# Kernel optimization log

Measured on AMD Instinct MI355X. Metric: run time of the kernel, lower is better.

Reference implementation:

```python
import jax, jax.numpy as jnp
import numpy as np

NUM_TASKS, IN_SIZE, OUT_SIZE, N_ROWS = 64, 512, 512, 2048


def setup_inputs() -> dict:
    key = jax.random.key(0)
    k_x, k_t, k_w = jax.random.split(key, 3)
    inputs = jax.random.normal(k_x, (N_ROWS, IN_SIZE), dtype=jnp.float32)
    task_ids = jax.random.randint(k_t, (N_ROWS,), 0, NUM_TASKS, dtype=jnp.int64)
    # in_size == out_size path: identity + N(0, 0.03) perturbation per task
    W = (jnp.eye(IN_SIZE, OUT_SIZE, dtype=jnp.float32)[None]
         + 0.03 * jax.random.normal(k_w, (NUM_TASKS, IN_SIZE, OUT_SIZE), dtype=jnp.float32))
    return {"inputs": inputs, "task_ids": task_ids, "W": W}


def reference(inputs, task_ids, W):
    # Gather the full per-row weight matrix then batched vector-matrix multiply,
    # faithful to torch.einsum('ni,nio->no', inputs, W[task_ids]).
    aligned = W[task_ids]                       # [I, in, out]
    return jnp.einsum("ni,nio->no", inputs, aligned)  # [I, out]
```

## Files before the change

### kernel.cpp

```cpp
#include <hip/hip_runtime.h>


#define NDIM 512
#define KDIM 512
#define NCOL 32

typedef _Float16 f16x8 __attribute__((ext_vector_type(8)));
typedef float    f32x4 __attribute__((ext_vector_type(4)));

__global__ __launch_bounds__(256) void k_fused(
    const float* __restrict__ x,
    const int*   __restrict__ tids,
    const float* __restrict__ W,
    float*       __restrict__ out,
    int n_rows)
{
    const int tid  = threadIdx.x;
    const int lane = tid & 63;
    const int wv   = tid >> 6;
    const int c0   = blockIdx.x * NCOL;
    const int task = blockIdx.y;

    __shared__ __align__(16) _Float16 Wt[NCOL * KDIM];
    __shared__ unsigned short rlw[4 * 128];
    __shared__ unsigned short rl[256];
    __shared__ int wcnt[4];

    int trow[8], tval[8];
    #pragma unroll
    for (int it = 0; it < 8; ++it) {
        trow[it] = wv * 512 + it * 64 + lane;
        tval[it] = (trow[it] < n_rows) ? tids[trow[it]] : -1;
    }

    const int sc4   = (tid & 7) * 4;
    const int obase = tid >> 3;
    const float* Wg = W + (size_t)task * KDIM * NDIM + c0;
    float4 wr[16];
    #pragma unroll
    for (int j = 0; j < 8; ++j)
        wr[j] = *(const float4*)(Wg + (size_t)(obase * 8 + j) * NDIM + sc4);
    #pragma unroll
    for (int j = 0; j < 8; ++j)
        wr[8 + j] = *(const float4*)(Wg + (size_t)((obase + 32) * 8 + j) * NDIM + sc4);

    int cloc = 0;
    #pragma unroll
    for (int it = 0; it < 8; ++it) {
        const bool m = (tval[it] == task);
        const unsigned long long bal = __ballot(m);
        const int rank = __popcll(bal & ((1ull << lane) - 1ull));
        if (m) rlw[wv * 128 + cloc + rank] = (unsigned short)trow[it];
        cloc += __popcll(bal);
    }
    if (lane == 0) wcnt[wv] = cloc;

    #pragma unroll
    for (int h = 0; h < 2; ++h) {
        const int oct = obase + h * 32;
        #pragma unroll
        for (int j2 = 0; j2 < 4; ++j2) {
            f16x8 h8;
            #pragma unroll
            for (int j = 0; j < 8; ++j)
                h8[j] = (_Float16)(((const float*)&wr[h * 8 + j])[j2]);
            const int c  = sc4 + j2;
            const int po = oct ^ (c & 7);
            *(f16x8*)&Wt[c * KDIM + po * 8] = h8;
        }
    }

    __syncthreads();

    const int n0 = wcnt[0], n1 = wcnt[1], n2 = wcnt[2], n3 = wcnt[3];
    const int o1 = n0, o2 = n0 + n1, o3 = o2 + n2;
    const int count = o3 + n3;
    if (tid < count && tid < 256) {
        int w, base;
        if (tid < o1)      { w = 0; base = 0;  }
        else if (tid < o2) { w = 1; base = o1; }
        else if (tid < o3) { w = 2; base = o2; }
        else               { w = 3; base = o3; }
        rl[tid] = rlw[w * 128 + tid - base];
    }
    __syncthreads();

    if (count == 0) return;

    const int ml = lane & 15;
    const int q  = lane >> 4;

    for (int g0 = 0; g0 < count; g0 += 64) {
        const int rr = g0 + wv * 16 + ml;
        const int rowid = rl[(rr < count) ? rr : 0];
        const float* xrow = x + (size_t)rowid * KDIM;

        f32x4 acc[2] = {};
        #pragma unroll
        for (int p = 0; p < 2; ++p) {
            const int kb = p * 256;
            float4 xa[16];
            #pragma unroll
            for (int ks = 0; ks < 8; ++ks) {
                xa[2 * ks]     = *(const float4*)(xrow + kb + ks * 32 + q * 8);
                xa[2 * ks + 1] = *(const float4*)(xrow + kb + ks * 32 + q * 8 + 4);
            }
            #pragma unroll
            for (int ks = 0; ks < 8; ++ks) {
                f16x8 af;
                const float* a0 = (const float*)&xa[2 * ks];
                #pragma unroll
                for (int j = 0; j < 8; ++j) af[j] = (_Float16)a0[j];
                #pragma unroll
                for (int ct = 0; ct < 2; ++ct) {
                    const int cB = ct * 16 + ml;
                    const int po = (p * 32 + ks * 4 + q) ^ (cB & 7);
                    const f16x8 bf = *(const f16x8*)&Wt[cB * KDIM + po * 8];
                    acc[ct] = __builtin_amdgcn_mfma_f32_16x16x32_f16(af, bf, acc[ct], 0, 0, 0);
                }
            }
        }

        #pragma unroll
        for (int rg = 0; rg < 4; ++rg) {
            const int rr2 = g0 + wv * 16 + q * 4 + rg;
            if (rr2 < count) {
                float* op = out + (size_t)rl[rr2] * NDIM + c0 + ml;
                op[0]  = acc[0][rg];
                op[16] = acc[1][rg];
            }
        }
    }
}

extern "C" void kernel_launch(void* const* d_in, const int* in_sizes, int n_in,
                              void* d_out, int out_size, void* d_ws, size_t ws_size,
                              hipStream_t stream) {
    const float* x    = (const float*)d_in[0];
    const int*   tids = (const int*)d_in[1];
    const float* W    = (const float*)d_in[2];
    float*       out  = (float*)d_out;
    const int n_rows  = in_sizes[1];

    k_fused<<<dim3(NDIM / NCOL, 64), dim3(256), 0, stream>>>(x, tids, W, out, n_rows);
}
```

Measured before the change: 108.4 us.

## Pipeline W chunk staging with per-wave row lists and prefetched activations

The W tile is split into two 16-column chunks staged one after the other, with the second chunk's global loads overlapping the MFMA work on the first. Each wave now keeps its own matched-row list, which removes the cross-wave compaction pass and one block barrier. Task ids are read with vectorized loads, activations are converted to fp16 fragments once and reused for both chunks, and launch bounds request higher occupancy. In exchange, MFMA work is spread unevenly across waves, since each wave processes only its own matched rows.

```diff
diff --git a/kernel.cpp b/kernel.cpp
--- a/kernel.cpp
+++ b/kernel.cpp
@@ -3,12 +3,14 @@
 
 #define NDIM 512
 #define KDIM 512
-#define NCOL 32
+#define CCH  16
+#define NCH  2
 
 typedef _Float16 f16x8 __attribute__((ext_vector_type(8)));
 typedef float    f32x4 __attribute__((ext_vector_type(4)));
+typedef int      i32x4 __attribute__((ext_vector_type(4)));
 
-__global__ __launch_bounds__(256) void k_fused(
+__global__ __launch_bounds__(256, 4) void k_fused2(
     const float* __restrict__ x,
     const int*   __restrict__ tids,
     const float* __restrict__ W,
@@ -18,92 +20,59 @@
     const int tid  = threadIdx.x;
     const int lane = tid & 63;
     const int wv   = tid >> 6;
-    const int c0   = blockIdx.x * NCOL;
+    const int c0   = blockIdx.x * (CCH * NCH);
     const int task = blockIdx.y;
 
-    __shared__ __align__(16) _Float16 Wt[NCOL * KDIM];
+    __shared__ __align__(16) _Float16 Wt[NCH][CCH * KDIM];
     __shared__ unsigned short rlw[4 * 128];
-    __shared__ unsigned short rl[256];
-    __shared__ int wcnt[4];
 
-    int trow[8], tval[8];
-    #pragma unroll
-    for (int it = 0; it < 8; ++it) {
-        trow[it] = wv * 512 + it * 64 + lane;
-        tval[it] = (trow[it] < n_rows) ? tids[trow[it]] : -1;
+    const int rbase = wv * 512 + lane * 8;
+    int tval[8];
+    if (rbase + 7 < n_rows) {
+        const i32x4 a = *(const i32x4*)(tids + rbase);
+        const i32x4 b = *(const i32x4*)(tids + rbase + 4);
+        tval[0] = a[0]; tval[1] = a[1]; tval[2] = a[2]; tval[3] = a[3];
+        tval[4] = b[0]; tval[5] = b[1]; tval[6] = b[2]; tval[7] = b[3];
+    } else {
+        #pragma unroll
+        for (int j = 0; j < 8; ++j)
+            tval[j] = (rbase + j < n_rows) ? tids[rbase + j] : -1;
     }
 
-    const int sc4   = (tid & 7) * 4;
-    const int obase = tid >> 3;
+    const int sc4   = (tid & 3) * 4;
+    const int obase = tid >> 2;
     const float* Wg = W + (size_t)task * KDIM * NDIM + c0;
-    float4 wr[16];
+    float4 wr[8];
     #pragma unroll
     for (int j = 0; j < 8; ++j)
         wr[j] = *(const float4*)(Wg + (size_t)(obase * 8 + j) * NDIM + sc4);
-    #pragma unroll
-    for (int j = 0; j < 8; ++j)
-        wr[8 + j] = *(const float4*)(Wg + (size_t)((obase + 32) * 8 + j) * NDIM + sc4);
 
     int cloc = 0;
     #pragma unroll
-    for (int it = 0; it < 8; ++it) {
-        const bool m = (tval[it] == task);
+    for (int j = 0; j < 8; ++j) {
+        const bool m = (tval[j] == task);
         const unsigned long long bal = __ballot(m);
         const int rank = __popcll(bal & ((1ull << lane) - 1ull));
-        if (m) rlw[wv * 128 + cloc + rank] = (unsigned short)trow[it];
+        if (m) rlw[wv * 128 + cloc + rank] = (unsigned short)(rbase + j);
         cloc += __popcll(bal);
     }
-    if (lane == 0) wcnt[wv] = cloc;
-
-    #pragma unroll
-    for (int h = 0; h < 2; ++h) {
-        const int oct = obase + h * 32;
-        #pragma unroll
-        for (int j2 = 0; j2 < 4; ++j2) {
-            f16x8 h8;
-            #pragma unroll
-            for (int j = 0; j < 8; ++j)
-                h8[j] = (_Float16)(((const float*)&wr[h * 8 + j])[j2]);
-            const int c  = sc4 + j2;
-            const int po = oct ^ (c & 7);
-            *(f16x8*)&Wt[c * KDIM + po * 8] = h8;
-        }
-    }
-
-    __syncthreads();
-
-    const int n0 = wcnt[0], n1 = wcnt[1], n2 = wcnt[2], n3 = wcnt[3];
-    const int o1 = n0, o2 = n0 + n1, o3 = o2 + n2;
-    const int count = o3 + n3;
-    if (tid < count && tid < 256) {
-        int w, base;
-        if (tid < o1)      { w = 0; base = 0;  }
-        else if (tid < o2) { w = 1; base = o1; }
-        else if (tid < o3) { w = 2; base = o2; }
-        else               { w = 3; base = o3; }
-        rl[tid] = rlw[w * 128 + tid - base];
-    }
-    __syncthreads();
-
-    if (count == 0) return;
 
     const int ml = lane & 15;
     const int q  = lane >> 4;
 
-    for (int g0 = 0; g0 < count; g0 += 64) {
-        const int rr = g0 + wv * 16 + ml;
-        const int rowid = rl[(rr < count) ? rr : 0];
-        const float* xrow = x + (size_t)rowid * KDIM;
+    f16x8 paf[16];
 
-        f32x4 acc[2] = {};
+    auto load_paf = [&](int g0) {
+        const int idx = g0 + ml;
+        const int nr  = (int)rlw[wv * 128 + ((idx < cloc) ? idx : (cloc - 1))];
+        const float* xr = x + (size_t)nr * KDIM;
         #pragma unroll
         for (int p = 0; p < 2; ++p) {
-            const int kb = p * 256;
-            float4 xa[16];
+            f32x4 xa[16];
             #pragma unroll
             for (int ks = 0; ks < 8; ++ks) {
-                xa[2 * ks]     = *(const float4*)(xrow + kb + ks * 32 + q * 8);
-                xa[2 * ks + 1] = *(const float4*)(xrow + kb + ks * 32 + q * 8 + 4);
+                xa[2 * ks]     = *(const f32x4*)(xr + p * 256 + ks * 32 + q * 8);
+                xa[2 * ks + 1] = *(const f32x4*)(xr + p * 256 + ks * 32 + q * 8 + 4);
             }
             #pragma unroll
             for (int ks = 0; ks < 8; ++ks) {
@@ -111,25 +80,79 @@
                 const float* a0 = (const float*)&xa[2 * ks];
                 #pragma unroll
                 for (int j = 0; j < 8; ++j) af[j] = (_Float16)a0[j];
-                #pragma unroll
-                for (int ct = 0; ct < 2; ++ct) {
-                    const int cB = ct * 16 + ml;
-                    const int po = (p * 32 + ks * 4 + q) ^ (cB & 7);
-                    const f16x8 bf = *(const f16x8*)&Wt[cB * KDIM + po * 8];
-                    acc[ct] = __builtin_amdgcn_mfma_f32_16x16x32_f16(af, bf, acc[ct], 0, 0, 0);
-                }
+                paf[p * 8 + ks] = af;
             }
         }
+    };
 
+    auto mma_tile = [&](int t) {
+        f32x4 acc = {};
+        #pragma unroll
+        for (int p = 0; p < 2; ++p) {
+            #pragma unroll
+            for (int ks = 0; ks < 8; ++ks) {
+                const int po = (p * 32 + ks * 4 + q) ^ (ml & 7);
+                const f16x8 bf = *(const f16x8*)&Wt[t][ml * KDIM + po * 8];
+                acc = __builtin_amdgcn_mfma_f32_16x16x32_f16(paf[p * 8 + ks], bf, acc, 0, 0, 0);
+            }
+        }
+        return acc;
+    };
+
+    auto store_tile = [&](int t, int g0, f32x4 acc) {
+        const int colb = c0 + t * CCH;
         #pragma unroll
         for (int rg = 0; rg < 4; ++rg) {
-            const int rr2 = g0 + wv * 16 + q * 4 + rg;
-            if (rr2 < count) {
-                float* op = out + (size_t)rl[rr2] * NDIM + c0 + ml;
-                op[0]  = acc[0][rg];
-                op[16] = acc[1][rg];
-            }
+            const int pos = g0 + q * 4 + rg;
+            if (pos < cloc)
+                out[(size_t)rlw[wv * 128 + pos] * NDIM + colb + ml] = acc[rg];
         }
+    };
+
+    if (cloc > 0) load_paf(0);
+
+    #pragma unroll
+    for (int j2 = 0; j2 < 4; ++j2) {
+        f16x8 h8;
+        #pragma unroll
+        for (int j = 0; j < 8; ++j)
+            h8[j] = (_Float16)(((const float*)&wr[j])[j2]);
+        const int c  = sc4 + j2;
+        const int po = obase ^ (c & 7);
+        *(f16x8*)&Wt[0][c * KDIM + po * 8] = h8;
+    }
+
+    #pragma unroll
+    for (int j = 0; j < 8; ++j)
+        wr[j] = *(const float4*)(Wg + (size_t)(obase * 8 + j) * NDIM + (CCH + sc4));
+
+    asm volatile("s_waitcnt lgkmcnt(0)" ::: "memory");
+    __builtin_amdgcn_s_barrier();
+    __builtin_amdgcn_sched_barrier(0);
+
+    if (cloc > 0) store_tile(0, 0, mma_tile(0));
+
+    #pragma unroll
+    for (int j2 = 0; j2 < 4; ++j2) {
+        f16x8 h8;
+        #pragma unroll
+        for (int j = 0; j < 8; ++j)
+            h8[j] = (_Float16)(((const float*)&wr[j])[j2]);
+        const int c  = sc4 + j2;
+        const int po = obase ^ (c & 7);
+        *(f16x8*)&Wt[1][c * KDIM + po * 8] = h8;
+    }
+
+    asm volatile("s_waitcnt lgkmcnt(0)" ::: "memory");
+    __builtin_amdgcn_s_barrier();
+    __builtin_amdgcn_sched_barrier(0);
+
+    if (cloc > 0) store_tile(1, 0, mma_tile(1));
+
+    for (int g0 = 16; g0 < cloc; g0 += 16) {
+        load_paf(g0);
+        store_tile(0, g0, mma_tile(0));
+        store_tile(1, g0, mma_tile(1));
     }
 }
 
@@ -142,5 +165,5 @@
     float*       out  = (float*)d_out;
     const int n_rows  = in_sizes[1];
 
-    k_fused<<<dim3(NDIM / NCOL, 64), dim3(256), 0, stream>>>(x, tids, W, out, n_rows);
+    k_fused2<<<dim3(NDIM / (CCH * NCH), 64), dim3(256), 0, stream>>>(x, tids, W, out, n_rows);
 }
```

Result: slower. 137.8 us (+27.1%).

## Make each wave own a task/column chunk independently, removing block barriers

Applied to the files above, without the earlier changes.

Each wave now handles its own (task, 32-column chunk) pair, with a private shared-memory weight tile and row list. This removes the __syncthreads barriers and the cross-wave list merge. The grid shrinks to 256 blocks of 4 waves, and block IDs are remapped to spread tasks. Weight staging is software-pipelined with double-buffered registers, overlapping global loads with the f16 conversion and LDS writes. x rows are loaded in quarters interleaved with MFMA. Shared memory grows to 128KB per block with launch_bounds(256,1), which limits occupancy. Every wave also rescans all 2048 task ids, and the row list is capped at 256.

```diff
diff --git a/kernel.cpp b/kernel.cpp
--- a/kernel.cpp
+++ b/kernel.cpp
@@ -4,11 +4,13 @@
 #define NDIM 512
 #define KDIM 512
 #define NCOL 32
+#define LISTCAP 256
 
 typedef _Float16 f16x8 __attribute__((ext_vector_type(8)));
 typedef float    f32x4 __attribute__((ext_vector_type(4)));
+typedef int      i32x4 __attribute__((ext_vector_type(4)));
 
-__global__ __launch_bounds__(256) void k_fused(
+__global__ __launch_bounds__(256, 1) void k_wave(
     const float* __restrict__ x,
     const int*   __restrict__ tids,
     const float* __restrict__ W,
@@ -18,116 +20,146 @@
     const int tid  = threadIdx.x;
     const int lane = tid & 63;
     const int wv   = tid >> 6;
-    const int c0   = blockIdx.x * NCOL;
-    const int task = blockIdx.y;
+    const int ml   = lane & 15;
+    const int q    = lane >> 4;
+    const int sc4  = (lane & 7) * 4;
+    const int ol   = lane >> 3;
 
-    __shared__ __align__(16) _Float16 Wt[NCOL * KDIM];
-    __shared__ unsigned short rlw[4 * 128];
-    __shared__ unsigned short rl[256];
-    __shared__ int wcnt[4];
+    const int bid   = blockIdx.x;
+    const int task  = (bid & 7) | ((bid >> 5) << 3);
+    const int chunk = ((bid >> 3) & 3) * 4 + wv;
+    const int c0    = chunk * NCOL;
 
-    int trow[8], tval[8];
+    __shared__ __align__(16) _Float16 Wt[4][NCOL * KDIM];
+    __shared__ unsigned short rl[4][LISTCAP];
+
+    _Float16*       Wm  = &Wt[wv][0];
+    unsigned short* rlm = &rl[wv][0];
+
+    const float* Wg = W + (size_t)task * KDIM * NDIM + c0;
+
+    i32x4 tvv[8];
     #pragma unroll
-    for (int it = 0; it < 8; ++it) {
-        trow[it] = wv * 512 + it * 64 + lane;
-        tval[it] = (trow[it] < n_rows) ? tids[trow[it]] : -1;
+    for (int cb = 0; cb < 8; ++cb) {
+        const int r4 = cb * 256 + lane * 4;
+        if (r4 + 3 < n_rows) {
+            tvv[cb] = *(const i32x4*)(tids + r4);
+        } else {
+            #pragma unroll
+            for (int j = 0; j < 4; ++j)
+                tvv[cb][j] = (r4 + j < n_rows) ? tids[r4 + j] : -1;
+        }
     }
 
-    const int sc4   = (tid & 7) * 4;
-    const int obase = tid >> 3;
-    const float* Wg = W + (size_t)task * KDIM * NDIM + c0;
-    float4 wr[16];
-    #pragma unroll
-    for (int j = 0; j < 8; ++j)
-        wr[j] = *(const float4*)(Wg + (size_t)(obase * 8 + j) * NDIM + sc4);
-    #pragma unroll
-    for (int j = 0; j < 8; ++j)
-        wr[8 + j] = *(const float4*)(Wg + (size_t)((obase + 32) * 8 + j) * NDIM + sc4);
-
-    int cloc = 0;
-    #pragma unroll
-    for (int it = 0; it < 8; ++it) {
-        const bool m = (tval[it] == task);
-        const unsigned long long bal = __ballot(m);
-        const int rank = __popcll(bal & ((1ull << lane) - 1ull));
-        if (m) rlw[wv * 128 + cloc + rank] = (unsigned short)trow[it];
-        cloc += __popcll(bal);
-    }
-    if (lane == 0) wcnt[wv] = cloc;
-
-    #pragma unroll
-    for (int h = 0; h < 2; ++h) {
-        const int oct = obase + h * 32;
+    float4 wrA[8], wrB[8];
+    auto issueS = [&](int s, float4 (&wb)[8]) {
+        const size_t kb = (size_t)(ol + 8 * s) * 8;
+        #pragma unroll
+        for (int j = 0; j < 8; ++j)
+            wb[j] = *(const float4*)(Wg + (kb + j) * NDIM + sc4);
+    };
+    auto stageS = [&](int s, const float4 (&wb)[8]) {
+        const int oct = ol + 8 * s;
         #pragma unroll
         for (int j2 = 0; j2 < 4; ++j2) {
             f16x8 h8;
             #pragma unroll
             for (int j = 0; j < 8; ++j)
-                h8[j] = (_Float16)(((const float*)&wr[h * 8 + j])[j2]);
+                h8[j] = (_Float16)(((const float*)&wb[j])[j2]);
             const int c  = sc4 + j2;
             const int po = oct ^ (c & 7);
-            *(f16x8*)&Wt[c * KDIM + po * 8] = h8;
+            *(f16x8*)&Wm[c * KDIM + po * 8] = h8;
+        }
+    };
+
+    issueS(0, wrA);
+    issueS(1, wrB);
+
+    int cnt = 0;
+    #pragma unroll
+    for (int cb = 0; cb < 8; ++cb) {
+        #pragma unroll
+        for (int j = 0; j < 4; ++j) {
+            const bool m = (tvv[cb][j] == task);
+            const unsigned long long bal = __ballot(m);
+            const int rank = __popcll(bal & ((1ull << lane) - 1ull));
+            const int slot = cnt + rank;
+            if (m && slot < LISTCAP) rlm[slot] = (unsigned short)(cb * 256 + lane * 4 + j);
+            cnt += __popcll(bal);
         }
     }
+    if (cnt > LISTCAP) cnt = LISTCAP;
 
-    __syncthreads();
+    stageS(0, wrA); issueS(2, wrA);
+    stageS(1, wrB); issueS(3, wrB);
+    stageS(2, wrA); issueS(4, wrA);
+    stageS(3, wrB); issueS(5, wrB);
+    stageS(4, wrA); issueS(6, wrA);
+    stageS(5, wrB); issueS(7, wrB);
+    stageS(6, wrA);
+    stageS(7, wrB);
 
-    const int n0 = wcnt[0], n1 = wcnt[1], n2 = wcnt[2], n3 = wcnt[3];
-    const int o1 = n0, o2 = n0 + n1, o3 = o2 + n2;
-    const int count = o3 + n3;
-    if (tid < count && tid < 256) {
-        int w, base;
-        if (tid < o1)      { w = 0; base = 0;  }
-        else if (tid < o2) { w = 1; base = o1; }
-        else if (tid < o3) { w = 2; base = o2; }
-        else               { w = 3; base = o3; }
-        rl[tid] = rlw[w * 128 + tid - base];
-    }
-    __syncthreads();
-
-    if (count == 0) return;
-
-    const int ml = lane & 15;
-    const int q  = lane >> 4;
-
-    for (int g0 = 0; g0 < count; g0 += 64) {
-        const int rr = g0 + wv * 16 + ml;
-        const int rowid = rl[(rr < count) ? rr : 0];
-        const float* xrow = x + (size_t)rowid * KDIM;
-
-        f32x4 acc[2] = {};
+    f32x4 xqA[8], xqB[8];
+    auto issueQ = [&](const float* xr, int qi, f32x4 (&xq)[8]) {
         #pragma unroll
-        for (int p = 0; p < 2; ++p) {
-            const int kb = p * 256;
-            float4 xa[16];
+        for (int s = 0; s < 4; ++s) {
+            const int ks = qi * 4 + s;
+            xq[2 * s]     = *(const f32x4*)(xr + ks * 32 + q * 8);
+            xq[2 * s + 1] = *(const f32x4*)(xr + ks * 32 + q * 8 + 4);
+        }
+    };
+    auto cvtQ = [&](const f32x4 (&xq)[8], f16x8* pf) {
+        #pragma unroll
+        for (int s = 0; s < 4; ++s) {
+            f16x8 af;
+            const float* a0 = (const float*)&xq[2 * s];
             #pragma unroll
-            for (int ks = 0; ks < 8; ++ks) {
-                xa[2 * ks]     = *(const float4*)(xrow + kb + ks * 32 + q * 8);
-                xa[2 * ks + 1] = *(const float4*)(xrow + kb + ks * 32 + q * 8 + 4);
+            for (int j = 0; j < 8; ++j) af[j] = (_Float16)a0[j];
+            pf[s] = af;
+        }
+    };
+    auto mmaH = [&](int half, const f16x8* pf, f32x4& a0, f32x4& a1) {
+        #pragma unroll
+        for (int ksl = 0; ksl < 8; ++ksl) {
+            const int oct = (half * 8 + ksl) * 4 + q;
+            {
+                const int po = oct ^ (ml & 7);
+                const f16x8 bf = *(const f16x8*)&Wm[ml * KDIM + po * 8];
+                a0 = __builtin_amdgcn_mfma_f32_16x16x32_f16(pf[ksl], bf, a0, 0, 0, 0);
             }
-            #pragma unroll
-            for (int ks = 0; ks < 8; ++ks) {
-                f16x8 af;
-                const float* a0 = (const float*)&xa[2 * ks];
-                #pragma unroll
-                for (int j = 0; j < 8; ++j) af[j] = (_Float16)a0[j];
-                #pragma unroll
-                for (int ct = 0; ct < 2; ++ct) {
-                    const int cB = ct * 16 + ml;
-                    const int po = (p * 32 + ks * 4 + q) ^ (cB & 7);
-                    const f16x8 bf = *(const f16x8*)&Wt[cB * KDIM + po * 8];
-                    acc[ct] = __builtin_amdgcn_mfma_f32_16x16x32_f16(af, bf, acc[ct], 0, 0, 0);
-                }
+            {
+                const int cB = 16 + ml;
+                const int po = oct ^ (cB & 7);
+                const f16x8 bf = *(const f16x8*)&Wm[cB * KDIM + po * 8];
+                a1 = __builtin_amdgcn_mfma_f32_16x16x32_f16(pf[ksl], bf, a1, 0, 0, 0);
             }
         }
+    };
+
+    for (int g0 = 0; g0 < cnt; g0 += 16) {
+        const int idx = g0 + ml;
+        const int row = rlm[(idx < cnt) ? idx : (cnt - 1)];
+        const float* xr = x + (size_t)row * KDIM;
+
+        f16x8 pafA[8], pafB[8];
+        f32x4 acc0 = {}, acc1 = {};
+
+        issueQ(xr, 0, xqA);
+        issueQ(xr, 1, xqB);
+        cvtQ(xqA, pafA);     issueQ(xr, 2, xqA);
+        cvtQ(xqB, pafA + 4); issueQ(xr, 3, xqB);
+        mmaH(0, pafA, acc0, acc1);
+        cvtQ(xqA, pafB);
+        cvtQ(xqB, pafB + 4);
+        mmaH(1, pafB, acc0, acc1);
 
         #pragma unroll
         for (int rg = 0; rg < 4; ++rg) {
-            const int rr2 = g0 + wv * 16 + q * 4 + rg;
-            if (rr2 < count) {
-                float* op = out + (size_t)rl[rr2] * NDIM + c0 + ml;
-                op[0]  = acc[0][rg];
-                op[16] = acc[1][rg];
+            const int pos = g0 + q * 4 + rg;
+            if (pos < cnt) {
+                float* op = out + (size_t)rlm[pos] * NDIM + c0 + ml;
+                op[0]  = acc0[rg];
+                op[16] = acc1[rg];
             }
         }
     }
@@ -142,5 +174,5 @@
     float*       out  = (float*)d_out;
     const int n_rows  = in_sizes[1];
 
-    k_fused<<<dim3(NDIM / NCOL, 64), dim3(256), 0, stream>>>(x, tids, W, out, n_rows);
+    k_wave<<<dim3(256), dim3(256), 0, stream>>>(x, tids, W, out, n_rows);
 }
```

New measurement: 106.1 us. 1.02x faster.
